# Performance work log

Hardware: AMD Instinct MI355X
Metric: run time of the kernel (lower is better)

Reference implementation:

```python
import jax, jax.numpy as jnp
import numpy as np

B, T, F, H = 4, 2048, 1024, 16
DK = F // H


def setup_inputs() -> dict:
    key = jax.random.key(0)
    ks = jax.random.split(key, 11)
    s = float(np.sqrt(1.0 / F))
    u = lambda k, shape: jax.random.uniform(k, shape, jnp.float32, -s, s)
    return {
        "query": jax.random.normal(ks[0], (B, T, F), jnp.float32),
        "key": jax.random.normal(ks[1], (B, T, F), jnp.float32),
        "value": jax.random.normal(ks[2], (B, T, F), jnp.float32),
        "mask": jnp.ones((B, 1, T), dtype=bool),
        "Wq": u(ks[3], (F, F)), "bq": u(ks[4], (F,)),
        "Wk": u(ks[5], (F, F)), "bk": u(ks[6], (F,)),
        "Wv": u(ks[7], (F, F)), "bv": u(ks[8], (F,)),
        "Wo": u(ks[9], (F, F)),
    }


def reference(query, key, value, mask, Wq, bq, Wk, bk, Wv, bv, Wo):
    b, t1, f = query.shape
    # project and split heads: (B, H, T, DK)
    q = (query @ Wq + bq).reshape(b, -1, H, DK).transpose(0, 2, 1, 3)
    k = (key @ Wk + bk).reshape(b, -1, H, DK).transpose(0, 2, 1, 3)
    v = (value @ Wv + bv).reshape(b, -1, H, DK).transpose(0, 2, 1, 3)
    # scaled dot-product scores (B, H, T1, T2)
    scores = jnp.einsum("bhqd,bhkd->bhqk", q, k) / jnp.sqrt(jnp.float32(DK))
    m = mask[:, None]  # (B, 1, 1|T1, T2)
    scores = jnp.where(m, scores, jnp.finfo(scores.dtype).min)
    attn = jax.nn.softmax(scores, axis=-1)
    attn = jnp.where(m, attn, 0.0)
    x = jnp.einsum("bhqk,bhkd->bhqd", attn, v)
    x = x.transpose(0, 2, 1, 3).reshape(b, t1, H * DK)
    return x @ Wo
```

## Files before the change

### kernel.cpp

```cpp
#include <hip/hip_runtime.h>
#include <hip/hip_bf16.h>
#include <math.h>

#define B_  4
#define T_  2048
#define F_  1024
#define H_  16

typedef short short8  __attribute__((ext_vector_type(8)));
typedef float f32x4   __attribute__((ext_vector_type(4)));
typedef float f32x16  __attribute__((ext_vector_type(16)));

__device__ __forceinline__ short f2bf(float f) {
  __hip_bfloat16 h = __float2bfloat16(f);
  short s;
  __builtin_memcpy(&s, &h, 2);
  return s;
}

__device__ __forceinline__ unsigned cvt_pk_bf16(float lo, float hi) {
  unsigned r;
  asm("v_cvt_pk_bf16_f32 %0, %1, %2" : "=v"(r) : "v"(lo), "v"(hi));
  return r;
}

__device__ __forceinline__ void gload_lds16(const void* g, void* l) {
  __builtin_amdgcn_global_load_lds(
      (const __attribute__((address_space(1))) void*)g,
      (__attribute__((address_space(3))) void*)l, 16, 0, 0);
}

__global__ __launch_bounds__(256) void k_cvt_bf16(const float* __restrict__ in,
                                                  short* __restrict__ out) {
  size_t i = ((size_t)blockIdx.x * 256 + threadIdx.x) * 8;
  float4 a = *(const float4*)(in + i);
  float4 b = *(const float4*)(in + i + 4);
  short8 o;
  o[0] = f2bf(a.x); o[1] = f2bf(a.y); o[2] = f2bf(a.z); o[3] = f2bf(a.w);
  o[4] = f2bf(b.x); o[5] = f2bf(b.y); o[6] = f2bf(b.z); o[7] = f2bf(b.w);
  *(short8*)(out + i) = o;
}

__global__ __launch_bounds__(256) void k_transpose(const float* __restrict__ W,
                                                   short* __restrict__ Wt) {
  __shared__ float t[64][65];
  const int x  = threadIdx.x & 63;
  const int y0 = threadIdx.x >> 6;
  const int n0 = blockIdx.x * 64;
  const int k0 = blockIdx.y * 64;
#pragma unroll
  for (int i = 0; i < 16; ++i) {
    int r = y0 * 16 + i;
    t[r][x] = W[(size_t)(k0 + r) * F_ + n0 + x];
  }
  __syncthreads();
#pragma unroll
  for (int i = 0; i < 16; ++i) {
    int r = y0 * 16 + i;
    Wt[(size_t)(n0 + r) * F_ + k0 + x] = f2bf(t[x][r]);
  }
}

__global__ __launch_bounds__(256) void k_vt(const short* __restrict__ Vp,
                                            short* __restrict__ Vt) {
  __shared__ short t[64][72];
  const int tid = threadIdx.x;
  const int tt = blockIdx.x * 64;
  const int h = blockIdx.y, b = blockIdx.z;
#pragma unroll
  for (int it = 0; it < 2; ++it) {
    int e = (tid + it * 256) * 8;
    int r = e >> 6, c = e & 63;
    *(short8*)&t[r][c] = *(const short8*)&Vp[(size_t)(b * T_ + tt + r) * F_ + h * 64 + c];
  }
  __syncthreads();
#pragma unroll
  for (int it = 0; it < 2; ++it) {
    int e = (tid + it * 256) * 8;
    int dr = e >> 6, tc = e & 63;
    short8 o;
#pragma unroll
    for (int j = 0; j < 8; ++j) o[j] = t[tc + j][dr];
    *(short8*)&Vt[((size_t)(b * H_ + h) * 64 + dr) * T_ + tt + tc] = o;
  }
}

template<int HAS_BIAS, int OUT_BF16>
__global__ __launch_bounds__(256) void k_gemm_bt(const short* __restrict__ A,
                                                 const short* __restrict__ Bt,
                                                 const float* __restrict__ bias,
                                                 void* __restrict__ Cout,
                                                 int M, int N, int K, float oscale) {
  __shared__ short aLds[2][128 * 32];
  __shared__ short bLds[2][128 * 32];
  const int tid = threadIdx.x;
  const int w = tid >> 6, l = tid & 63;
  const int lr = l & 15, lg = l >> 4;
  const int p = blockIdx.x;
  const int L = (p & 7) * ((int)gridDim.x >> 3) + (p >> 3);
  const int rowBase = (L >> 3) * 128;
  const int colBase = (L & 7) * 128;
  const int wrow = (w >> 1) * 64, wcol = (w & 1) * 64;
  f32x4 acc[4][4] = {};

  auto STAGE = [&](int bufi, int kt) {
#pragma unroll
    for (int s2 = 0; s2 < 2; ++s2) {
      int c   = w * 2 + s2;
      int row = c * 16 + (l >> 2);
      int kk  = (l & 3) * 8;
      gload_lds16(A  + (size_t)(rowBase + row) * K + kt + kk, (char*)&aLds[bufi][0] + c * 1024);
      gload_lds16(Bt + (size_t)(colBase + row) * K + kt + kk, (char*)&bLds[bufi][0] + c * 1024);
    }
  };

  STAGE(0, 0);
  __syncthreads();
  int buf = 0;
  for (int kt = 0; kt < K; kt += 32) {
    if (kt + 32 < K) STAGE(buf ^ 1, kt + 32);
    short8 af[4], bf[4];
#pragma unroll
    for (int m = 0; m < 4; ++m)
      af[m] = *(const short8*)&aLds[buf][(wrow + m * 16 + lr) * 32 + lg * 8];
#pragma unroll
    for (int n = 0; n < 4; ++n)
      bf[n] = *(const short8*)&bLds[buf][(wcol + n * 16 + lr) * 32 + lg * 8];
#pragma unroll
    for (int m = 0; m < 4; ++m)
#pragma unroll
      for (int n = 0; n < 4; ++n)
        acc[m][n] = __builtin_amdgcn_mfma_f32_16x16x32_bf16(af[m], bf[n], acc[m][n], 0, 0, 0);
    __syncthreads();
    buf ^= 1;
  }

  float bv[4];
#pragma unroll
  for (int n = 0; n < 4; ++n)
    bv[n] = HAS_BIAS ? bias[colBase + wcol + n * 16 + lr] : 0.f;
#pragma unroll
  for (int m = 0; m < 4; ++m)
#pragma unroll
    for (int n = 0; n < 4; ++n) {
      int col = colBase + wcol + n * 16 + lr;
#pragma unroll
      for (int r = 0; r < 4; ++r) {
        int row = rowBase + wrow + m * 16 + lg * 4 + r;
        float v = (acc[m][n][r] + bv[n]) * oscale;
        if (OUT_BF16) ((short*)Cout)[(size_t)row * N + col] = f2bf(v);
        else          ((float*)Cout)[(size_t)row * N + col] = v;
      }
    }
}

__global__ __launch_bounds__(256) void k_flash(const short* __restrict__ Qp,
                                               const short* __restrict__ Kp,
                                               const short* __restrict__ Vt,
                                               short* __restrict__ Xp) {
  __shared__ __align__(16) short kLds[2][64 * 64];
  __shared__ __align__(16) short vLds[2][64 * 64];
  const int tid = threadIdx.x, w = tid >> 6, l = tid & 63;
  const int lo = l & 31, hi = l >> 5;
  const int p = blockIdx.x;
  const int L = (p & 7) * 128 + (p >> 3);
  const int bh = L >> 4, qblk = L & 15;
  const int b = bh >> 4;
  const int hbase = (bh & 15) * 64;
  const int qw0 = b * T_ + qblk * 128 + w * 32;
  const int kvrow0 = b * T_;
  const short* Vb = Vt + (size_t)bh * 64 * T_;

  short8 aq[4];
#pragma unroll
  for (int ds = 0; ds < 4; ++ds)
    aq[ds] = *(const short8*)&Qp[(size_t)(qw0 + lo) * F_ + hbase + ds * 16 + hi * 8];

  short8 ones;
#pragma unroll
  for (int j = 0; j < 8; ++j) ones[j] = (short)0x3F80;

  const short* kSrc[2];
  const short* vSrc[2];
#pragma unroll
  for (int i = 0; i < 2; ++i) {
    int s = (w * 2 + i) * 64 + l;
    int srow = s >> 3;
    int schunk = ((s & 7) ^ (srow & 7)) * 8;
    kSrc[i] = Kp + (size_t)(kvrow0 + srow) * F_ + hbase + schunk;
    vSrc[i] = Vb + (size_t)srow * T_ + schunk;
  }

  auto STAGE = [&](int bufi) {
#pragma unroll
    for (int i = 0; i < 2; ++i) {
      gload_lds16(kSrc[i], (char*)(&kLds[bufi][0]) + (w * 2 + i) * 1024);
      gload_lds16(vSrc[i], (char*)(&vLds[bufi][0]) + (w * 2 + i) * 1024);
      kSrc[i] += 64 * F_;
      vSrc[i] += 64;
    }
  };

  f32x16 acc[2] = {};
  f32x16 acc_l = {};

  STAGE(0);
  __syncthreads();

  int buf = 0;
  for (int kt = 0; kt < T_; kt += 64) {
    if (kt + 64 < T_) STAGE(buf ^ 1);

    f32x16 s[2] = {};
    __builtin_amdgcn_s_setprio(1);
#pragma unroll
    for (int ds = 0; ds < 4; ++ds)
#pragma unroll
      for (int st = 0; st < 2; ++st) {
        int row = st * 32 + lo;
        short8 kf = *(const short8*)((char*)(&kLds[buf][0]) + row * 128 +
                                     (((2 * ds + hi) ^ (row & 7)) * 16));
        s[st] = __builtin_amdgcn_mfma_f32_32x32x16_bf16(kf, aq[ds], s[st], 0, 0, 0);
      }
    __builtin_amdgcn_s_setprio(0);

#pragma unroll
    for (int st = 0; st < 2; ++st)
#pragma unroll
      for (int r = 0; r < 16; ++r)
        s[st][r] = __builtin_amdgcn_exp2f(s[st][r]);

    short8 pa[4];
#pragma unroll
    for (int st = 0; st < 2; ++st)
#pragma unroll
      for (int half = 0; half < 2; ++half) {
        const int g0 = 2 * half, g1 = 2 * half + 1;
        unsigned A0 = cvt_pk_bf16(s[st][4 * g0 + 0], s[st][4 * g0 + 1]);
        unsigned A1 = cvt_pk_bf16(s[st][4 * g0 + 2], s[st][4 * g0 + 3]);
        unsigned B0 = cvt_pk_bf16(s[st][4 * g1 + 0], s[st][4 * g1 + 1]);
        unsigned B1 = cvt_pk_bf16(s[st][4 * g1 + 2], s[st][4 * g1 + 3]);
        asm volatile("v_permlane32_swap_b32 %0, %1" : "+v"(A0), "+v"(B0));
        asm volatile("v_permlane32_swap_b32 %0, %1" : "+v"(A1), "+v"(B1));
        uint4 u4 = {A0, A1, B0, B1};
        pa[st * 2 + half] = *(short8*)&u4;
      }

    __builtin_amdgcn_s_setprio(1);
#pragma unroll
    for (int ks = 0; ks < 4; ++ks) {
#pragma unroll
      for (int dsub = 0; dsub < 2; ++dsub) {
        int row = dsub * 32 + lo;
        short8 vf = *(const short8*)((char*)(&vLds[buf][0]) + row * 128 +
                                     (((2 * ks + hi) ^ (row & 7)) * 16));
        acc[dsub] = __builtin_amdgcn_mfma_f32_32x32x16_bf16(pa[ks], vf, acc[dsub], 0, 0, 0);
      }
      acc_l = __builtin_amdgcn_mfma_f32_32x32x16_bf16(pa[ks], ones, acc_l, 0, 0, 0);
    }
    __builtin_amdgcn_s_setprio(0);

    __syncthreads();
    buf ^= 1;
  }

#pragma unroll
  for (int dsub = 0; dsub < 2; ++dsub)
#pragma unroll
    for (int r = 0; r < 16; ++r) {
      int qr = (r & 3) + 8 * (r >> 2) + 4 * hi;
      Xp[(size_t)(qw0 + qr) * F_ + hbase + dsub * 32 + lo] =
          f2bf(acc[dsub][r] / acc_l[r]);
    }
}

extern "C" void kernel_launch(void* const* d_in, const int* in_sizes, int n_in,
                              void* d_out, int out_size, void* d_ws, size_t ws_size,
                              hipStream_t stream) {
  const float* query = (const float*)d_in[0];
  const float* key   = (const float*)d_in[1];
  const float* value = (const float*)d_in[2];
  const float* Wq = (const float*)d_in[4];
  const float* bq = (const float*)d_in[5];
  const float* Wk = (const float*)d_in[6];
  const float* bk = (const float*)d_in[7];
  const float* Wv = (const float*)d_in[8];
  const float* bv = (const float*)d_in[9];
  const float* Wo = (const float*)d_in[10];
  float* out = (float*)d_out;

  const size_t MB = 1u << 20;
  char* ws = (char*)d_ws;
  short* qb  = (short*)(ws +   0 * MB);
  short* kb  = (short*)(ws +  16 * MB);
  short* vb  = (short*)(ws +  32 * MB);
  short* WqT = (short*)(ws +  48 * MB);
  short* WkT = (short*)(ws +  50 * MB);
  short* WvT = (short*)(ws +  52 * MB);
  short* WoT = (short*)(ws +  54 * MB);
  short* Qp  = (short*)(ws +  56 * MB);
  short* Kp  = (short*)(ws +  72 * MB);
  short* Vp  = (short*)(ws +  88 * MB);
  short* Xp  = qb;
  short* Vt  = vb;

  const int NTOK = B_ * T_;
  dim3 blk(256);
  dim3 gcv(NTOK * F_ / 8 / 256);
  k_cvt_bf16<<<gcv, blk, 0, stream>>>(query, qb);
  k_cvt_bf16<<<gcv, blk, 0, stream>>>(key,   kb);
  k_cvt_bf16<<<gcv, blk, 0, stream>>>(value, vb);
  dim3 gtr(16, 16);
  k_transpose<<<gtr, blk, 0, stream>>>(Wq, WqT);
  k_transpose<<<gtr, blk, 0, stream>>>(Wk, WkT);
  k_transpose<<<gtr, blk, 0, stream>>>(Wv, WvT);
  k_transpose<<<gtr, blk, 0, stream>>>(Wo, WoT);
  const int NG = (NTOK / 128) * (F_ / 128);
  const float qscale = 0.125f * 1.44269504f;
  k_gemm_bt<1, 1><<<NG, blk, 0, stream>>>(qb, WqT, bq, Qp, NTOK, F_, F_, qscale);
  k_gemm_bt<1, 1><<<NG, blk, 0, stream>>>(kb, WkT, bk, Kp, NTOK, F_, F_, 1.0f);
  k_gemm_bt<1, 1><<<NG, blk, 0, stream>>>(vb, WvT, bv, Vp, NTOK, F_, F_, 1.0f);
  k_vt<<<dim3(T_ / 64, H_, B_), blk, 0, stream>>>(Vp, Vt);
  k_flash<<<(T_ / 128) * B_ * H_, blk, 0, stream>>>(Qp, Kp, Vt, Xp);
  k_gemm_bt<0, 0><<<NG, blk, 0, stream>>>(Xp, WoT, nullptr, out, NTOK, F_, F_, 1.0f);
}
```

Before: 261.6 us.

## Register-stage K/V tiles with two-deep prefetch in flash kernel; merge cvt launches

The flash-attention loop no longer uses direct global-to-LDS loads. It loads the K/V tiles into registers two iterations ahead and writes them to double-buffered LDS before each compute step, with a lighter lgkm wait plus barrier in place of __syncthreads. This is meant to hide global memory latency behind the MFMA work while costing extra VGPRs and explicit LDS stores. The three fp32-to-bf16 conversion launches are also merged into one kernel to cut launch overhead.

```diff
diff --git a/kernel.cpp b/kernel.cpp
--- a/kernel.cpp
+++ b/kernel.cpp
@@ -30,9 +30,22 @@
       (__attribute__((address_space(3))) void*)l, 16, 0, 0);
 }
 
-__global__ __launch_bounds__(256) void k_cvt_bf16(const float* __restrict__ in,
-                                                  short* __restrict__ out) {
-  size_t i = ((size_t)blockIdx.x * 256 + threadIdx.x) * 8;
+__device__ __forceinline__ void barrier_lgkm() {
+  asm volatile("s_waitcnt lgkmcnt(0)" ::: "memory");
+  __builtin_amdgcn_sched_barrier(0);
+  __builtin_amdgcn_s_barrier();
+}
+
+__global__ __launch_bounds__(256) void k_cvt3_bf16(const float* __restrict__ q,
+                                                   const float* __restrict__ k,
+                                                   const float* __restrict__ v,
+                                                   short* __restrict__ qo,
+                                                   short* __restrict__ ko,
+                                                   short* __restrict__ vo) {
+  const int seg = blockIdx.x >> 12;
+  const float* in  = seg == 0 ? q  : (seg == 1 ? k  : v);
+  short*       out = seg == 0 ? qo : (seg == 1 ? ko : vo);
+  size_t i = (((size_t)(blockIdx.x & 4095)) * 256 + threadIdx.x) * 8;
   float4 a = *(const float4*)(in + i);
   float4 b = *(const float4*)(in + i + 4);
   short8 o;
@@ -182,6 +195,7 @@
 
   const short* kSrc[2];
   const short* vSrc[2];
+  int ldsOff[2];
 #pragma unroll
   for (int i = 0; i < 2; ++i) {
     int s = (w * 2 + i) * 64 + l;
@@ -189,28 +203,29 @@
     int schunk = ((s & 7) ^ (srow & 7)) * 8;
     kSrc[i] = Kp + (size_t)(kvrow0 + srow) * F_ + hbase + schunk;
     vSrc[i] = Vb + (size_t)srow * T_ + schunk;
-  }
-
-  auto STAGE = [&](int bufi) {
-#pragma unroll
-    for (int i = 0; i < 2; ++i) {
-      gload_lds16(kSrc[i], (char*)(&kLds[bufi][0]) + (w * 2 + i) * 1024);
-      gload_lds16(vSrc[i], (char*)(&vLds[bufi][0]) + (w * 2 + i) * 1024);
-      kSrc[i] += 64 * F_;
-      vSrc[i] += 64;
-    }
-  };
+    ldsOff[i] = (w * 2 + i) * 1024 + l * 16;
+  }
+
+  short8 kA0, kA1, vA0, vA1;
+  short8 kB0, kB1, vB0, vB1;
+#define LOADSET(K0, K1, V0, V1)                                            \
+  do {                                                                     \
+    K0 = *(const short8*)kSrc[0]; K1 = *(const short8*)kSrc[1];            \
+    V0 = *(const short8*)vSrc[0]; V1 = *(const short8*)vSrc[1];            \
+    kSrc[0] += 64 * F_; kSrc[1] += 64 * F_; vSrc[0] += 64; vSrc[1] += 64;  \
+  } while (0)
+#define WRITESET(bufi, K0, K1, V0, V1)                                     \
+  do {                                                                     \
+    *(short8*)((char*)(&kLds[bufi][0]) + ldsOff[0]) = K0;                  \
+    *(short8*)((char*)(&kLds[bufi][0]) + ldsOff[1]) = K1;                  \
+    *(short8*)((char*)(&vLds[bufi][0]) + ldsOff[0]) = V0;                  \
+    *(short8*)((char*)(&vLds[bufi][0]) + ldsOff[1]) = V1;                  \
+  } while (0)
 
   f32x16 acc[2] = {};
   f32x16 acc_l = {};
 
-  STAGE(0);
-  __syncthreads();
-
-  int buf = 0;
-  for (int kt = 0; kt < T_; kt += 64) {
-    if (kt + 64 < T_) STAGE(buf ^ 1);
-
+  auto COMPUTE = [&](int bufi) {
     f32x16 s[2] = {};
     __builtin_amdgcn_s_setprio(1);
 #pragma unroll
@@ -218,7 +233,7 @@
 #pragma unroll
       for (int st = 0; st < 2; ++st) {
         int row = st * 32 + lo;
-        short8 kf = *(const short8*)((char*)(&kLds[buf][0]) + row * 128 +
+        short8 kf = *(const short8*)((char*)(&kLds[bufi][0]) + row * 128 +
                                      (((2 * ds + hi) ^ (row & 7)) * 16));
         s[st] = __builtin_amdgcn_mfma_f32_32x32x16_bf16(kf, aq[ds], s[st], 0, 0, 0);
       }
@@ -252,17 +267,31 @@
 #pragma unroll
       for (int dsub = 0; dsub < 2; ++dsub) {
         int row = dsub * 32 + lo;
-        short8 vf = *(const short8*)((char*)(&vLds[buf][0]) + row * 128 +
+        short8 vf = *(const short8*)((char*)(&vLds[bufi][0]) + row * 128 +
                                      (((2 * ks + hi) ^ (row & 7)) * 16));
         acc[dsub] = __builtin_amdgcn_mfma_f32_32x32x16_bf16(pa[ks], vf, acc[dsub], 0, 0, 0);
       }
       acc_l = __builtin_amdgcn_mfma_f32_32x32x16_bf16(pa[ks], ones, acc_l, 0, 0, 0);
     }
     __builtin_amdgcn_s_setprio(0);
-
-    __syncthreads();
-    buf ^= 1;
-  }
+  };
+
+  LOADSET(kA0, kA1, vA0, vA1);
+  LOADSET(kB0, kB1, vB0, vB1);
+  WRITESET(0, kA0, kA1, vA0, vA1);
+  barrier_lgkm();
+  for (int t = 0; t < 32; t += 2) {
+    if (t + 2 < 32) LOADSET(kA0, kA1, vA0, vA1);
+    WRITESET(1, kB0, kB1, vB0, vB1);
+    COMPUTE(0);
+    barrier_lgkm();
+    if (t + 3 < 32) LOADSET(kB0, kB1, vB0, vB1);
+    if (t + 2 < 32) WRITESET(0, kA0, kA1, vA0, vA1);
+    COMPUTE(1);
+    barrier_lgkm();
+  }
+#undef LOADSET
+#undef WRITESET
 
 #pragma unroll
   for (int dsub = 0; dsub < 2; ++dsub)
@@ -306,10 +335,7 @@
 
   const int NTOK = B_ * T_;
   dim3 blk(256);
-  dim3 gcv(NTOK * F_ / 8 / 256);
-  k_cvt_bf16<<<gcv, blk, 0, stream>>>(query, qb);
-  k_cvt_bf16<<<gcv, blk, 0, stream>>>(key,   kb);
-  k_cvt_bf16<<<gcv, blk, 0, stream>>>(value, vb);
+  k_cvt3_bf16<<<3 * 4096, blk, 0, stream>>>(query, key, value, qb, kb, vb);
   dim3 gtr(16, 16);
   k_transpose<<<gtr, blk, 0, stream>>>(Wq, WqT);
   k_transpose<<<gtr, blk, 0, stream>>>(Wk, WkT);
```

Result: faster. 255.0 us (-2.5%).
